# Performance work log

Hardware: AMD Instinct MI355X
Metric: run time of the kernel (lower is better)

Reference implementation:

```python
import jax, jax.numpy as jnp
import numpy as np

N = 100000   # nodes
D = 64       # node_emb_dim
R = 8        # num relations
E = 1600000  # edges (avg degree 16)


def setup_inputs() -> dict:
    key = jax.random.key(0)
    k1, k2, k3, k4, k5 = jax.random.split(key, 5)
    x = jax.random.normal(k1, (N, D), dtype=jnp.float32)
    edge_index = jax.random.randint(k2, (2, E), 0, N, dtype=jnp.int64)
    edge_type = jax.random.randint(k3, (E,), 0, R, dtype=jnp.int64)
    W_rel = jax.random.normal(k4, (R, D, D), dtype=jnp.float32) / np.sqrt(D)
    W_root = jax.random.normal(k5, (D, D), dtype=jnp.float32) / np.sqrt(D)
    bias = jnp.zeros((D,), dtype=jnp.float32)
    return {"x": x, "edge_index": edge_index, "edge_type": edge_type,
            "W_rel": W_rel, "W_root": W_root, "bias": bias}


def reference(x, edge_index, edge_type, W_rel, W_root, bias):
    # PyG RGCNConv: per-relation linear transform of source nodes,
    # mean-aggregated per (target node, relation), plus root transform + bias.
    n_nodes, d = x.shape
    n_rel = W_rel.shape[0]
    src, dst = edge_index[0], edge_index[1]

    # Transform every node under every relation once: [N, R, D]
    h_all = jnp.einsum('nd,rde->nre', x, W_rel)
    # Gather per-edge message: [E, D]
    msg = h_all[src, edge_type]

    # Per-(dst, relation) in-degree counts for mean normalization
    cnt = jnp.zeros((n_nodes, n_rel), dtype=x.dtype).at[dst, edge_type].add(1.0)
    norm = 1.0 / jnp.maximum(cnt[dst, edge_type], 1.0)  # [E]

    # Scatter-add normalized messages to target nodes
    agg = jnp.zeros((n_nodes, d), dtype=x.dtype).at[dst].add(msg * norm[:, None])

    out = agg + x @ W_root + bias
    return (out, edge_index, edge_type)
```

## Files before the change

kernel.cpp:

```cpp
#include <hip/hip_runtime.h>

#define DD 64
#define RR 8
#define KA 576
#define NT 18
#define NPART 8
#define ECH 2048
#define TILE 16
#define SEGCAP 160

typedef short bf16x8 __attribute__((ext_vector_type(8)));
typedef float f32x4  __attribute__((ext_vector_type(4)));

__device__ __forceinline__ float bf2f(unsigned short u) {
    union { unsigned u; float f; } c; c.u = ((unsigned)u) << 16; return c.f;
}
__device__ __forceinline__ unsigned short f2bf(float f) {
    union { float f; unsigned u; } c; c.f = f;
    unsigned u = c.u;
    u += 0x7FFF + ((u >> 16) & 1);
    return (unsigned short)(u >> 16);
}

__global__ __launch_bounds__(256) void k_front(
    const int* __restrict__ ei, const int* __restrict__ et,
    int* __restrict__ cnt, unsigned long long* __restrict__ q,
    int* __restrict__ qlen, float* __restrict__ out_ei,
    float* __restrict__ out_et, int E, unsigned pmagic,
    const float* __restrict__ x, unsigned short* __restrict__ xb,
    const float* __restrict__ Wrel, const float* __restrict__ Wroot,
    unsigned short* __restrict__ Bh, int N, int nsb, int xblocks)
{
    if ((int)blockIdx.x >= nsb) {
        int pb = (int)blockIdx.x - nsb;
        if (pb < xblocks) {
            int i = pb * 256 + threadIdx.x;
            int total = (N + 1) * (DD / 4);
            if (i >= total) return;
            ushort4 o;
            if (i < N * (DD / 4)) {
                float4 f = ((const float4*)x)[i];
                o = make_ushort4(f2bf(f.x), f2bf(f.y), f2bf(f.z), f2bf(f.w));
            } else {
                o = make_ushort4(0, 0, 0, 0);
            }
            ((ushort4*)xb)[i] = o;
        } else {
            int idx = (pb - xblocks) * 256 + threadIdx.x;
            if (idx >= NT * 4 * 64 * 8) return;
            int i    = idx & 7;
            int lane = (idx >> 3) & 63;
            int f    = (idx >> 9) & 3;
            int t    = idx >> 11;
            int k = t * 32 + (lane >> 4) * 8 + i;
            int d = f * 16 + (lane & 15);
            int r = k >> 6, kk = k & 63;
            float w = (r < RR) ? Wrel[((size_t)r * DD + kk) * DD + d]
                               : Wroot[(size_t)kk * DD + d];
            Bh[idx] = f2bf(w);
        }
        return;
    }

    const int base = blockIdx.x * ECH + threadIdx.x;
    const int lane = threadIdx.x & 63;
    const int gwid = blockIdx.x * 4 + (threadIdx.x >> 6);

    int d[8], t[8], s[8], rk[8]; bool m[8];
    #pragma unroll
    for (int j = 0; j < 8; ++j) {
        int e = base + j * 256;
        m[j] = (e < E);
        d[j] = m[j] ? ei[E + e] : 0;
    }
    #pragma unroll
    for (int j = 0; j < 8; ++j) {
        int e = base + j * 256;
        if (m[j]) { t[j] = et[e]; s[j] = ei[e]; }
    }
    #pragma unroll
    for (int j = 0; j < 8; ++j)
        if (m[j]) rk[j] = atomicAdd(&cnt[(size_t)d[j] * RR + t[j]], 1);
    #pragma unroll
    for (int j = 0; j < 8; ++j) {
        int e = base + j * 256;
        if (m[j]) {
            out_ei[e]     = (float)s[j];
            out_ei[E + e] = (float)d[j];
            out_et[e]     = (float)t[j];
        }
    }

    int run0=0,run1=0,run2=0,run3=0,run4=0,run5=0,run6=0,run7=0;
    unsigned long long* qw = q + (size_t)gwid * NPART * SEGCAP;
    #pragma unroll
    for (int j = 0; j < 8; ++j) {
        int pj = m[j]
            ? (int)(((unsigned long long)(unsigned)d[j] * pmagic) >> 32)
            : -1;
        unsigned long long k0 = __ballot(pj == 0);
        unsigned long long k1 = __ballot(pj == 1);
        unsigned long long k2 = __ballot(pj == 2);
        unsigned long long k3 = __ballot(pj == 3);
        unsigned long long k4 = __ballot(pj == 4);
        unsigned long long k5 = __ballot(pj == 5);
        unsigned long long k6 = __ballot(pj == 6);
        unsigned long long k7 = __ballot(pj == 7);
        unsigned long long km =
            (pj==0)?k0:(pj==1)?k1:(pj==2)?k2:(pj==3)?k3:
            (pj==4)?k4:(pj==5)?k5:(pj==6)?k6:k7;
        int bb =
            (pj==0)?run0:(pj==1)?run1:(pj==2)?run2:(pj==3)?run3:
            (pj==4)?run4:(pj==5)?run5:(pj==6)?run6:run7;
        int off = __popcll(km & ((1ull << lane) - 1ull));
        if (pj >= 0 && bb + off < SEGCAP) {
            unsigned lo = (unsigned)s[j] | ((unsigned)t[j]  << 20);
            unsigned hi = (unsigned)d[j] | ((unsigned)rk[j] << 20);
            qw[(size_t)pj * SEGCAP + bb + off] =
                ((unsigned long long)hi << 32) | lo;
        }
        run0 += __popcll(k0); run1 += __popcll(k1);
        run2 += __popcll(k2); run3 += __popcll(k3);
        run4 += __popcll(k4); run5 += __popcll(k5);
        run6 += __popcll(k6); run7 += __popcll(k7);
    }
    if (lane == 0) {
        int* ql = qlen + (size_t)gwid * NPART;
        ql[0]=run0; ql[1]=run1; ql[2]=run2; ql[3]=run3;
        ql[4]=run4; ql[5]=run5; ql[6]=run6; ql[7]=run7;
    }
}

__global__ __launch_bounds__(256) void k_alloc(
    const int* __restrict__ cnt, int* __restrict__ startv,
    int* __restrict__ start2, int* __restrict__ counter,
    int* __restrict__ sorted, int N)
{
    __shared__ int sdata[256];
    __shared__ int sbase;
    const int tid = threadIdx.x;
    const int n = blockIdx.x * 256 + tid;

    int deg = 0, deg8 = 0;
    int c[RR];
    if (n < N) {
        const int4* c4 = (const int4*)(cnt + (size_t)n * RR);
        int4 a = c4[0], b = c4[1];
        c[0]=a.x; c[1]=a.y; c[2]=a.z; c[3]=a.w;
        c[4]=b.x; c[5]=b.y; c[6]=b.z; c[7]=b.w;
        #pragma unroll
        for (int r = 0; r < RR; ++r) deg += c[r];
        deg8 = (deg + 7) & ~7;
    }
    sdata[tid] = deg8;
    __syncthreads();
    int v = deg8;
    #pragma unroll
    for (int off = 1; off < 256; off <<= 1) {
        int t = (tid >= off) ? sdata[tid - off] : 0;
        __syncthreads();
        v += t;
        sdata[tid] = v;
        __syncthreads();
    }
    if (tid == 255) sbase = atomicAdd(counter, v);
    __syncthreads();
    if (n < N) {
        int st = sbase + v - deg8;
        startv[n] = st;
        int h = st;
        #pragma unroll
        for (int r = 0; r < RR; ++r) { start2[(size_t)n * RR + r] = h; h += c[r]; }
        for (int j = deg; j < deg8; ++j) sorted[st + j] = N;
    }
}

__global__ __launch_bounds__(256) void k_scatter_seg(
    const unsigned long long* __restrict__ q, const int* __restrict__ qlen,
    const int* __restrict__ start2, int* __restrict__ sorted, int nwaves)
{
    const int p    = blockIdx.x & (NPART - 1);
    const int grp  = blockIdx.x / NPART;
    const int gwid = grp * 4 + (threadIdx.x >> 6);
    const int lane = threadIdx.x & 63;
    if (gwid >= nwaves) return;
    const int seg = gwid * NPART + p;
    const int len = qlen[seg];
    const unsigned long long* qs = q + (size_t)seg * SEGCAP;
    for (int i = lane; i < len; i += 64) {
        unsigned long long v = qs[i];
        int cell = (int)((v >> 32) & 0xFFFFFu) * RR + (int)((v >> 20) & 7u);
        int pos  = start2[cell] + (int)(v >> 52);
        sorted[pos] = (int)(v & 0xFFFFFu);
    }
}

__global__ __launch_bounds__(256) void k_agg_mfma(
    const unsigned short* __restrict__ xb, const int* __restrict__ sorted,
    const int* __restrict__ startv, const int* __restrict__ cnt,
    const unsigned short* __restrict__ Bh, const float* __restrict__ bias,
    float* __restrict__ out, int N)
{
    __shared__ __align__(16) unsigned short As[TILE * KA];
    const int nb   = blockIdx.x * TILE;
    const int wv   = threadIdx.x >> 6;
    const int lane = threadIdx.x & 63;

    const int row0 = wv * 4;
    const int dst0 = nb + row0;
    const int nv   = min(4, N - dst0);
    if (nv > 0) {
        int cidx = lane & 31;
        if (cidx >= nv * 8) cidx = nv * 8 - 1;
        const int cv = cnt[(size_t)dst0 * RR + cidx];
        int sidx = lane & 3;
        if (sidx >= nv) sidx = nv - 1;
        const int sv = startv[dst0 + sidx];

        for (int i = 0; i < 4; ++i) {
            if (i >= nv) break;
            const int row = row0 + i;
            const int dst = dst0 + i;
            const int xsh = (row & 7) << 3;
            unsigned short* ao = As + row * KA;
            const int cb = i * 8;

            int deg = 0;
            #pragma unroll
            for (int r = 0; r < RR; ++r)
                deg += __builtin_amdgcn_readlane(cv, cb + r);
            const int deg8 = (deg + 7) & ~7;

            const int s0  = __builtin_amdgcn_readlane(sv, i);
            const int end = s0 + deg8;

            int   r      = 0;
            int   c_r    = __builtin_amdgcn_readlane(cv, cb);
            int   next_b = s0 + c_r;
            float cur    = 0.f;

            auto flush = [&]() {
                float inv = __builtin_amdgcn_rcpf(fmaxf((float)c_r, 1.f));
                ao[(r * DD + lane) ^ xsh] = f2bf(cur * inv);
                cur = 0.f;
                ++r;
                c_r = __builtin_amdgcn_readlane(cv, cb + (r & 7));
                next_b += c_r;
            };

            int e = s0;
            int wbase = s0;
            int vidx  = sorted[wbase + lane];
            while (e < end) {
                if (e - wbase >= 64) {
                    wbase = e;
                    vidx  = sorted[wbase + lane];
                }
                const int k    = e - wbase;
                const int take = min(end - e, 64 - k);
                for (int ii = 0; ii < take; ii += 8) {
                    int q0 = __builtin_amdgcn_readlane(vidx, k + ii + 0);
                    int q1 = __builtin_amdgcn_readlane(vidx, k + ii + 1);
                    int q2 = __builtin_amdgcn_readlane(vidx, k + ii + 2);
                    int q3 = __builtin_amdgcn_readlane(vidx, k + ii + 3);
                    int q4 = __builtin_amdgcn_readlane(vidx, k + ii + 4);
                    int q5 = __builtin_amdgcn_readlane(vidx, k + ii + 5);
                    int q6 = __builtin_amdgcn_readlane(vidx, k + ii + 6);
                    int q7 = __builtin_amdgcn_readlane(vidx, k + ii + 7);
                    unsigned short u0 = xb[(size_t)q0 * DD + lane];
                    unsigned short u1 = xb[(size_t)q1 * DD + lane];
                    unsigned short u2 = xb[(size_t)q2 * DD + lane];
                    unsigned short u3 = xb[(size_t)q3 * DD + lane];
                    unsigned short u4 = xb[(size_t)q4 * DD + lane];
                    unsigned short u5 = xb[(size_t)q5 * DD + lane];
                    unsigned short u6 = xb[(size_t)q6 * DD + lane];
                    unsigned short u7 = xb[(size_t)q7 * DD + lane];
                    const int base = e + ii;
                    while (base + 0 == next_b && r < RR) flush();
                    cur += bf2f(u0);
                    while (base + 1 == next_b && r < RR) flush();
                    cur += bf2f(u1);
                    while (base + 2 == next_b && r < RR) flush();
                    cur += bf2f(u2);
                    while (base + 3 == next_b && r < RR) flush();
                    cur += bf2f(u3);
                    while (base + 4 == next_b && r < RR) flush();
                    cur += bf2f(u4);
                    while (base + 5 == next_b && r < RR) flush();
                    cur += bf2f(u5);
                    while (base + 6 == next_b && r < RR) flush();
                    cur += bf2f(u6);
                    while (base + 7 == next_b && r < RR) flush();
                    cur += bf2f(u7);
                }
                e += take;
            }
            while (r < RR) flush();

            ao[(8 * DD + lane) ^ xsh] = xb[(size_t)dst * DD + lane];
        }
    }

    __syncthreads();

    const int rlo = lane & 15;
    const int kg  = lane >> 4;
    const int cf  = wv;
    const int row = rlo;
    const int xsh = (row & 7) << 3;

    f32x4 acc = {0.f,0.f,0.f,0.f};

    const unsigned short* arow = As + row * KA;
    #pragma unroll
    for (int t = 0; t < NT; ++t) {
        bf16x8 a = *(const bf16x8*)(arow + ((t * 32 + kg * 8) ^ xsh));
        bf16x8 b = *(const bf16x8*)(Bh + (size_t)t * 2048 + (size_t)cf * 512
                                       + lane * 8);
        acc = __builtin_amdgcn_mfma_f32_16x16x32_bf16(a, b, acc, 0, 0, 0);
    }

    const float bl = bias[rlo + cf * 16];
    const int orow = nb + kg * 4;
    #pragma unroll
    for (int j = 0; j < 4; ++j) {
        int rr2 = orow + j;
        if (rr2 < N) out[(size_t)rr2 * DD + rlo + cf * 16] = acc[j] + bl;
    }
}

extern "C" void kernel_launch(void* const* d_in, const int* in_sizes, int n_in,
                              void* d_out, int out_size, void* d_ws, size_t ws_size,
                              hipStream_t stream)
{
    const float* x     = (const float*)d_in[0];
    const int*   ei    = (const int*)d_in[1];
    const int*   et    = (const int*)d_in[2];
    const float* Wrel  = (const float*)d_in[3];
    const float* Wroot = (const float*)d_in[4];
    const float* bias  = (const float*)d_in[5];

    const int N = in_sizes[0] / DD;
    const int E = in_sizes[2];
    const int M = N * RR;

    float* out    = (float*)d_out;
    float* out_ei = out + (size_t)N * DD;
    float* out_et = out_ei + (size_t)2 * E;

    auto align = [](size_t v) { return (v + 255) & ~(size_t)255; };

    const int nsb    = (E + ECH - 1) / ECH;
    const int nwaves = nsb * 4;
    const int ngrp   = (nwaves + 3) / 4;

    size_t p = 0;
    int* cnt = (int*)((char*)d_ws + p);              p += align((size_t)M * 4);
    int* counter = (int*)((char*)d_ws + p);
    size_t zero_bytes = p + 256;                     p += 256;
    int* startv = (int*)((char*)d_ws + p);           p += align((size_t)N * 4);
    int* start2 = (int*)((char*)d_ws + p);           p += align((size_t)M * 4);
    unsigned long long* q = (unsigned long long*)((char*)d_ws + p);
    p += align((size_t)nwaves * NPART * SEGCAP * 8);
    int* qlen = (int*)((char*)d_ws + p);             p += align((size_t)nwaves * NPART * 4);
    int* sorted = (int*)((char*)d_ws + p);           p += align(((size_t)E + 7*(size_t)N + 128) * 4);
    unsigned short* xb = (unsigned short*)((char*)d_ws + p); p += align(((size_t)N + 1) * DD * 2);
    unsigned short* Bh = (unsigned short*)((char*)d_ws + p); p += align((size_t)NT*4*64*8*2);

    hipMemsetAsync(d_ws, 0, zero_bytes, stream);

    unsigned pmagic = (unsigned)((((unsigned long long)NPART << 32) + N - 1) / N);

    const int xblocks = ((N + 1) * (DD / 4) + 255) / 256;
    const int wblocks = (NT * 4 * 64 * 8 + 255) / 256;

    k_front<<<dim3(nsb + xblocks + wblocks), 256, 0, stream>>>(
        ei, et, cnt, q, qlen, out_ei, out_et, E, pmagic,
        x, xb, Wrel, Wroot, Bh, N, nsb, xblocks);
    k_alloc<<<dim3((N + 255) / 256), 256, 0, stream>>>(
        cnt, startv, start2, counter, sorted, N);
    k_scatter_seg<<<dim3(ngrp * NPART), 256, 0, stream>>>(
        q, qlen, start2, sorted, nwaves);
    k_agg_mfma<<<dim3((N + TILE - 1) / TILE), 256, 0, stream>>>(
        xb, sorted, startv, cnt, Bh, bias, out, N);
}
```

Baseline: 192.7 us.

## Move per-(dst,relation) count atomics into a partition-grouped pass

Removes the random-address atomicAdd on the count array from the front edge pass and adds a new kernel that walks the destination-partitioned queues, doing the atomics there and writing each edge's rank back into its queue entry. Because each launch block handles one destination partition, its atomics hit a narrower address range, which is meant to improve cache locality. The cost is an extra kernel launch plus a re-read and rewrite of the queue buffer.

```diff
diff --git a/kernel.cpp b/kernel.cpp
--- a/kernel.cpp
+++ b/kernel.cpp
@@ -24,9 +24,9 @@
 
 __global__ __launch_bounds__(256) void k_front(
     const int* __restrict__ ei, const int* __restrict__ et,
-    int* __restrict__ cnt, unsigned long long* __restrict__ q,
-    int* __restrict__ qlen, float* __restrict__ out_ei,
-    float* __restrict__ out_et, int E, unsigned pmagic,
+    unsigned long long* __restrict__ q, int* __restrict__ qlen,
+    float* __restrict__ out_ei, float* __restrict__ out_et, int E,
+    unsigned pmagic,
     const float* __restrict__ x, unsigned short* __restrict__ xb,
     const float* __restrict__ Wrel, const float* __restrict__ Wroot,
     unsigned short* __restrict__ Bh, int N, int nsb, int xblocks)
@@ -66,7 +66,7 @@
     const int lane = threadIdx.x & 63;
     const int gwid = blockIdx.x * 4 + (threadIdx.x >> 6);
 
-    int d[8], t[8], s[8], rk[8]; bool m[8];
+    int d[8], t[8], s[8]; bool m[8];
     #pragma unroll
     for (int j = 0; j < 8; ++j) {
         int e = base + j * 256;
@@ -78,9 +78,6 @@
         int e = base + j * 256;
         if (m[j]) { t[j] = et[e]; s[j] = ei[e]; }
     }
-    #pragma unroll
-    for (int j = 0; j < 8; ++j)
-        if (m[j]) rk[j] = atomicAdd(&cnt[(size_t)d[j] * RR + t[j]], 1);
     #pragma unroll
     for (int j = 0; j < 8; ++j) {
         int e = base + j * 256;
@@ -114,8 +111,8 @@
             (pj==4)?run4:(pj==5)?run5:(pj==6)?run6:run7;
         int off = __popcll(km & ((1ull << lane) - 1ull));
         if (pj >= 0 && bb + off < SEGCAP) {
-            unsigned lo = (unsigned)s[j] | ((unsigned)t[j]  << 20);
-            unsigned hi = (unsigned)d[j] | ((unsigned)rk[j] << 20);
+            unsigned lo = (unsigned)s[j] | ((unsigned)t[j] << 20);
+            unsigned hi = (unsigned)d[j];
             qw[(size_t)pj * SEGCAP + bb + off] =
                 ((unsigned long long)hi << 32) | lo;
         }
@@ -128,6 +125,28 @@
         int* ql = qlen + (size_t)gwid * NPART;
         ql[0]=run0; ql[1]=run1; ql[2]=run2; ql[3]=run3;
         ql[4]=run4; ql[5]=run5; ql[6]=run6; ql[7]=run7;
+    }
+}
+
+__global__ __launch_bounds__(256) void k_count_seg(
+    unsigned long long* __restrict__ q, const int* __restrict__ qlen,
+    int* __restrict__ cnt, int nwaves)
+{
+    const int p    = blockIdx.x & (NPART - 1);
+    const int grp  = blockIdx.x / NPART;
+    const int gwid = grp * 4 + (threadIdx.x >> 6);
+    const int lane = threadIdx.x & 63;
+    if (gwid >= nwaves) return;
+    const int seg = gwid * NPART + p;
+    const int len = qlen[seg];
+    unsigned long long* qs = q + (size_t)seg * SEGCAP;
+    for (int i = lane; i < len; i += 64) {
+        unsigned long long v = qs[i];
+        unsigned hi   = (unsigned)(v >> 32);
+        unsigned rel  = (unsigned)(v >> 20) & 7u;
+        int cell = (int)(hi & 0xFFFFFu) * RR + (int)rel;
+        unsigned rank = (unsigned)atomicAdd(&cnt[cell], 1);
+        ((unsigned*)&qs[i])[1] = hi | (rank << 20);
     }
 }
 
@@ -375,8 +394,10 @@
     const int wblocks = (NT * 4 * 64 * 8 + 255) / 256;
 
     k_front<<<dim3(nsb + xblocks + wblocks), 256, 0, stream>>>(
-        ei, et, cnt, q, qlen, out_ei, out_et, E, pmagic,
+        ei, et, q, qlen, out_ei, out_et, E, pmagic,
         x, xb, Wrel, Wroot, Bh, N, nsb, xblocks);
+    k_count_seg<<<dim3(ngrp * NPART), 256, 0, stream>>>(
+        q, qlen, cnt, nwaves);
     k_alloc<<<dim3((N + 255) / 256), 256, 0, stream>>>(
         cnt, startv, start2, counter, sorted, N);
     k_scatter_seg<<<dim3(ngrp * NPART), 256, 0, stream>>>(
```

Measured after the change: 190.7 us. No clear change (-1.0%).
